# Kernel tuning notes

Measured on AMD Instinct MI355X. Metric: run time of the kernel, lower is better.

Reference implementation:

```python
import jax, jax.numpy as jnp
from jax import lax
import numpy as np

N_LAYERS = 2
HIDDEN = 1024
N_STOCKS = 1024
LB, UB = 0.0, 0.2
REBAL_ITERS = 32  # fixed upper bound; loop converges in 1-2 iters in practice


def setup_inputs() -> dict:
    key = jax.random.key(0)
    ks = jax.random.split(key, 20)
    B, T = 512, 128
    inp = {"x": jax.random.normal(ks[0], (B, T, N_STOCKS), dtype=jnp.float32)}
    k = 1
    for l in range(N_LAYERS):
        in_dim = N_STOCKS if l == 0 else HIDDEN
        s = 1.0 / np.sqrt(HIDDEN)
        inp[f"w_ih_{l}"] = jax.random.uniform(ks[k], (3 * HIDDEN, in_dim), minval=-s, maxval=s); k += 1
        inp[f"w_hh_{l}"] = jax.random.uniform(ks[k], (3 * HIDDEN, HIDDEN), minval=-s, maxval=s); k += 1
        inp[f"b_ih_{l}"] = jax.random.uniform(ks[k], (3 * HIDDEN,), minval=-s, maxval=s); k += 1
        inp[f"b_hh_{l}"] = jax.random.uniform(ks[k], (3 * HIDDEN,), minval=-s, maxval=s); k += 1
    s = 1.0 / np.sqrt(HIDDEN)
    inp["fc_w"] = jax.random.uniform(ks[k], (N_STOCKS, HIDDEN), minval=-s, maxval=s); k += 1
    inp["fc_b"] = jax.random.uniform(ks[k], (N_STOCKS,), minval=-s, maxval=s)
    return inp


def _gru_layer(x, w_ih, w_hh, b_ih, b_hh):
    # x: [B,T,D] -> hidden sequence [B,T,H]; PyTorch GRU cell math
    B, T, _ = x.shape
    H = w_hh.shape[1]
    x_proj = jnp.einsum('btd,gd->btg', x, w_ih) + b_ih  # [B,T,3H]

    def step(h, xp):
        hp = h @ w_hh.T + b_hh
        xr, xz, xn = jnp.split(xp, 3, axis=-1)
        hr, hz, hn = jnp.split(hp, 3, axis=-1)
        r = jax.nn.sigmoid(xr + hr)
        z = jax.nn.sigmoid(xz + hz)
        n = jnp.tanh(xn + r * hn)
        h_new = (1.0 - z) * n + z * h
        return h_new, h_new

    h0 = jnp.zeros((B, H), x.dtype)
    _, hs = lax.scan(step, h0, jnp.swapaxes(x_proj, 0, 1))  # [T,B,H]
    return jnp.swapaxes(hs, 0, 1)


def _rebalance(w, lb, ub, n_iters=REBAL_ITERS):
    # Batched version of the iterative capped-simplex redistribution loop.
    old = w
    wc = jnp.clip(w, lb, ub)
    done = jnp.zeros((w.shape[0],), dtype=bool)

    def body(state, _):
        old, wc, done = state
        leftover = jnp.sum(old - wc, axis=-1, keepdims=True)            # [B,1]
        mask = wc != ub                                                  # nominees
        num = jnp.sum(mask, axis=-1)                                     # [B]
        nom_sum = jnp.sum(jnp.where(mask, wc, 0.0), axis=-1, keepdims=True)
        gift = leftover * wc / jnp.where(nom_sum == 0.0, 1.0, nom_sum)
        wc_new = jnp.where(mask, wc + gift, wc)
        no_nom = num == 0
        over = jnp.any(wc_new > ub, axis=-1)
        new_done = done | no_nom | (~over)
        wc_next = jnp.where(no_nom[:, None], wc,
                            jnp.where(over[:, None], jnp.clip(wc_new, lb, ub), wc_new))
        old_next = jnp.where(no_nom[:, None], old, wc_new)
        wc_out = jnp.where(done[:, None], wc, wc_next)
        old_out = jnp.where(done[:, None], old, old_next)
        return (old_out, wc_out, new_done), None

    (_, wc, _), _ = lax.scan(body, (old, wc, done), None, length=n_iters)
    return wc


def reference(x, w_ih_0, w_hh_0, b_ih_0, b_hh_0, w_ih_1, w_hh_1, b_ih_1, b_hh_1, fc_w, fc_b):
    h = _gru_layer(x, w_ih_0, w_hh_0, b_ih_0, b_hh_0)
    h = _gru_layer(h, w_ih_1, w_hh_1, b_ih_1, b_hh_1)
    h_t = h[:, -1, :]                                   # last time step [B,H]
    logit = h_t @ fc_w.T + fc_b                         # dropout is identity in eval
    logit = jax.nn.silu(logit)
    probs = jax.nn.softmax(logit, axis=-1)
    return _rebalance(probs, LB, UB)
```

## Files before the change

### kernel.cpp

```cpp
#include <hip/hip_runtime.h>
#include <hip/hip_bf16.h>
#include <stdint.h>

#define BB 512
#define TT 128
#define DD 1024
#define HH 1024
#define G3 3072
#define TC 32
#define NCH (TT/TC)
#define NRING 33

typedef __bf16 bft;
typedef __bf16 bf16x8 __attribute__((ext_vector_type(8)));
typedef float f32x4 __attribute__((ext_vector_type(4)));

__device__ __forceinline__ void gl_lds16(const bft* g, void* lds_base_uniform) {
  __builtin_amdgcn_global_load_lds(
      (const __attribute__((address_space(1))) void*)g,
      (__attribute__((address_space(3))) void*)lds_base_uniform,
      16, 0, 0);
}

__device__ __forceinline__ void st_wt_bf16(bft* p, float v) {
  bft h = (bft)v;
  union { bft h; unsigned short u; } cv; cv.h = h;
  unsigned int uv = cv.u;
  asm volatile("global_store_short %0, %1, off sc0 sc1" :: "v"(p), "v"(uv) : "memory");
}
__device__ __forceinline__ void st_wt_f32(float* p, float v) {
  asm volatile("global_store_dword %0, %1, off sc0 sc1" :: "v"(p), "v"(v) : "memory");
}
__device__ __forceinline__ void st_wt_u32(int* p, int v) {
  asm volatile("global_store_dword %0, %1, off sc0 sc1" :: "v"(p), "v"(v) : "memory");
}
__device__ __forceinline__ int ld_co_u32(const int* p) {
  int v;
  asm volatile("global_load_dword %0, %1, off sc0 sc1\n\ts_waitcnt vmcnt(0)"
               : "=v"(v) : "v"(p) : "memory");
  return v;
}

__global__ void k_cvt(const float* __restrict__ in, bft* __restrict__ out, long n) {
  long i = ((long)blockIdx.x * blockDim.x + threadIdx.x) * 8;
  long stride = (long)gridDim.x * blockDim.x * 8;
  for (; i < n; i += stride) {
    float4 a = *(const float4*)(in + i);
    float4 b = *(const float4*)(in + i + 4);
    bf16x8 r;
    r[0] = (bft)a.x; r[1] = (bft)a.y; r[2] = (bft)a.z; r[3] = (bft)a.w;
    r[4] = (bft)b.x; r[5] = (bft)b.y; r[6] = (bft)b.z; r[7] = (bft)b.w;
    *(bf16x8*)(out + i) = r;
  }
}

template<int AMODE, int EPI>
__launch_bounds__(256)
__global__ void k_gemm(const void* __restrict__ Ap, long lda,
                       const bft* __restrict__ W, long ldw,
                       const float* __restrict__ bias,
                       void* __restrict__ Cout, long ldc,
                       int t0, int K) {
  __shared__ unsigned char sm[32768];
  const int tid  = threadIdx.x;
  const int lane = tid & 63;
  const int wid  = tid >> 6;
  const int m0 = blockIdx.y * 128;
  const int n0 = blockIdx.x * 128;
  const int wm = wid >> 1, wn = wid & 1;

  f32x4 acc[4][4] = {};

  for (int k0 = 0; k0 < K; k0 += 64) {
    if (AMODE == 1) {
      const float* Af = (const float*)Ap;
#pragma unroll
      for (int s = 0; s < 4; ++s) {
        int seg = wid * 4 + s;
        int row = seg * 8 + (lane >> 3);
        int mr = m0 + row;
        long grow = (long)(mr >> 5) * TT + t0 + (mr & 31);
        const float* src = Af + grow * lda + k0 + (lane & 7) * 8;
        float4 a  = *(const float4*)src;
        float4 b2 = *(const float4*)(src + 4);
        bf16x8 r;
        r[0] = (bft)a.x;  r[1] = (bft)a.y;  r[2] = (bft)a.z;  r[3] = (bft)a.w;
        r[4] = (bft)b2.x; r[5] = (bft)b2.y; r[6] = (bft)b2.z; r[7] = (bft)b2.w;
        *(bf16x8*)(sm + seg * 1024 + (lane >> 3) * 128 +
                   (((lane & 7) * 16) ^ ((row & 7) << 4))) = r;
      }
    } else {
      const bft* Ab = (const bft*)Ap;
#pragma unroll
      for (int s = 0; s < 4; ++s) {
        int seg = wid * 4 + s;
        int row = seg * 8 + (lane >> 3);
        int cbs = ((lane & 7) * 16) ^ ((row & 7) << 4);
        int mr = m0 + row;
        long grow;
        if (AMODE == 0) grow = mr;
        else { int sl = t0 + (mr & 31); if (sl >= NRING) sl -= NRING;
               grow = (long)sl * BB + (mr >> 5); }
        gl_lds16(Ab + grow * lda + k0 + (cbs >> 1), sm + seg * 1024);
      }
    }
#pragma unroll
    for (int s = 0; s < 4; ++s) {
      int seg = wid * 4 + s;
      int row = seg * 8 + (lane >> 3);
      int cbs = ((lane & 7) * 16) ^ ((row & 7) << 4);
      gl_lds16(W + (long)(n0 + row) * ldw + k0 + (cbs >> 1), sm + 16384 + seg * 1024);
    }
    __syncthreads();
#pragma unroll
    for (int ks = 0; ks < 2; ++ks) {
      int kb = ks * 64 + (lane >> 4) * 16;
      bf16x8 aF[4], bF[4];
#pragma unroll
      for (int mi = 0; mi < 4; ++mi) {
        int row = wm * 64 + mi * 16 + (lane & 15);
        aF[mi] = *(const bf16x8*)(sm + row * 128 + (kb ^ ((row & 7) << 4)));
      }
#pragma unroll
      for (int ni = 0; ni < 4; ++ni) {
        int row = wn * 64 + ni * 16 + (lane & 15);
        bF[ni] = *(const bf16x8*)(sm + 16384 + row * 128 + (kb ^ ((row & 7) << 4)));
      }
#pragma unroll
      for (int mi = 0; mi < 4; ++mi)
#pragma unroll
        for (int ni = 0; ni < 4; ++ni)
          acc[mi][ni] = __builtin_amdgcn_mfma_f32_16x16x32_bf16(aF[mi], bF[ni], acc[mi][ni], 0, 0, 0);
    }
    __syncthreads();
  }

#pragma unroll
  for (int mi = 0; mi < 4; ++mi)
#pragma unroll
    for (int ni = 0; ni < 4; ++ni) {
      int col = n0 + wn * 64 + ni * 16 + (lane & 15);
      float bv = bias[col];
#pragma unroll
      for (int r = 0; r < 4; ++r) {
        long row = m0 + wm * 64 + mi * 16 + (lane >> 4) * 4 + r;
        float v = acc[mi][ni][r] + bv;
        if (EPI == 0) {
          ((bft*)Cout)[row * ldc + col] = (bft)v;
        } else {
          ((float*)Cout)[row * ldc + col] = v / (1.f + expf(-v));
        }
      }
    }
}

__launch_bounds__(256, 1)
__global__ void k_persist(const bft* __restrict__ whh, const float* __restrict__ bhh,
                          const bft* __restrict__ xp,
                          bft* __restrict__ ring,
                          float* __restrict__ hfc, int* __restrict__ flags,
                          int t0s, int first, int pbase) {
  __shared__ unsigned char sm[163840];
  unsigned char* smW = sm;
  unsigned char* smA = sm + 98304;

  const int tid  = threadIdx.x;
  const int lane = tid & 63;
  const int wid  = tid >> 6;
  const int bid  = blockIdx.x;
  const int xcd = bid & 7, loc = bid >> 3;
  const int mt = xcd >> 1;
  const int nt = (xcd & 1) * 32 + loc;
  const int j0 = nt * 16;
  const int m0 = mt * 128;
  const int j  = j0 + (lane & 15);
  int* gflags = flags + mt * 64;

#pragma unroll
  for (int s8 = 0; s8 < 24; ++s8) {
    int s = wid * 24 + s8;
    int row = s >> 1;
    int half = s & 1;
    int hb = half * 1024 + lane * 16;
    int sb = hb ^ ((row & 7) << 4);
    long grow = (long)(row >> 4) * 1024 + j0 + (row & 15);
    gl_lds16(whh + grow * 1024 + (sb >> 1), smW + s * 1024);
  }
  asm volatile("s_waitcnt vmcnt(0)" ::: "memory");
  __builtin_amdgcn_s_barrier();

  const float br = bhh[j], bz = bhh[1024 + j], bn = bhh[2048 + j];

  auto stageA = [&](const bft* base, int k0, int bufsel) {
    unsigned char* dst = smA + bufsel * 16384;
#pragma unroll
    for (int si = 0; si < 4; ++si) {
      int seg = wid * 4 + si;
      int row = seg * 8 + (lane >> 3);
      int cb = ((lane & 7) * 16) ^ ((row & 7) << 4);
      gl_lds16(base + (long)(m0 + row) * DD + k0 + (cb >> 1), dst + seg * 1024);
    }
  };

  float xg[3][2][4];
  float hp[2][4];

  auto prefXG = [&](int s) {
#pragma unroll
    for (int mi = 0; mi < 2; ++mi)
#pragma unroll
      for (int r = 0; r < 4; ++r) {
        long b = m0 + wid * 32 + mi * 16 + (lane >> 4) * 4 + r;
        long xrow = (b * TC + s) * (long)G3 + j;
        xg[0][mi][r] = (float)xp[xrow];
        xg[1][mi][r] = (float)xp[xrow + 1024];
        xg[2][mi][r] = (float)xp[xrow + 2048];
      }
  };

  prefXG(0);
  if (first) {
#pragma unroll
    for (int mi = 0; mi < 2; ++mi)
#pragma unroll
      for (int r = 0; r < 4; ++r) hp[mi][r] = 0.f;
  } else {
#pragma unroll
    for (int mi = 0; mi < 2; ++mi)
#pragma unroll
      for (int r = 0; r < 4; ++r) {
        long b = m0 + wid * 32 + mi * 16 + (lane >> 4) * 4 + r;
        hp[mi][r] = hfc[b * HH + j];
      }
  }
  __builtin_amdgcn_sched_barrier(0);

  for (int s = 0; s < TC; ++s) {
    if (s) {
      int target = pbase + s;
      if (tid < 64) {
        const int* fp = gflags + tid;
        while (ld_co_u32(fp) < target) __builtin_amdgcn_s_sleep(2);
      }
      __syncthreads();
    }

    int sl = t0s + s; if (sl >= NRING) sl -= NRING;
    int psl = sl ? sl - 1 : NRING - 1;

    f32x4 acc[3][2] = {};
    if (!(first && s == 0)) {
      const bft* Ab = ring + (long)psl * (BB * (long)DD);
      stageA(Ab, 0, 0);
      stageA(Ab, 64, 1);
      stageA(Ab, 128, 2);
#pragma unroll
      for (int k = 0; k < 16; ++k) {
        __builtin_amdgcn_s_barrier();
        if (k < 13) stageA(Ab, (k + 3) * 64, (k + 3) & 3);
        if (k < 13)       asm volatile("s_waitcnt vmcnt(12)" ::: "memory");
        else if (k == 13) asm volatile("s_waitcnt vmcnt(8)" ::: "memory");
        else if (k == 14) asm volatile("s_waitcnt vmcnt(4)" ::: "memory");
        else              asm volatile("s_waitcnt vmcnt(0)" ::: "memory");
        __builtin_amdgcn_s_barrier();
        __builtin_amdgcn_sched_barrier(0);
        const unsigned char* Abuf = smA + (k & 3) * 16384;
#pragma unroll
        for (int ks = 0; ks < 2; ++ks) {
          int kb = ks * 64 + (lane >> 4) * 16;
          bf16x8 aF[2], bF[3];
#pragma unroll
          for (int mi = 0; mi < 2; ++mi) {
            int row = wid * 32 + mi * 16 + (lane & 15);
            aF[mi] = *(const bf16x8*)(Abuf + row * 128 + (kb ^ ((row & 7) << 4)));
          }
#pragma unroll
          for (int g = 0; g < 3; ++g) {
            int wrow = g * 16 + (lane & 15);
            bF[g] = *(const bf16x8*)(smW + wrow * 2048 + ((k * 128 + kb) ^ ((wrow & 7) << 4)));
          }
#pragma unroll
          for (int g = 0; g < 3; ++g)
#pragma unroll
            for (int mi = 0; mi < 2; ++mi)
              acc[g][mi] = __builtin_amdgcn_mfma_f32_16x16x32_bf16(aF[mi], bF[g], acc[g][mi], 0, 0, 0);
        }
      }
    }

    bft* outp = ring + (long)sl * (BB * (long)DD);
#pragma unroll
    for (int mi = 0; mi < 2; ++mi)
#pragma unroll
      for (int r = 0; r < 4; ++r) {
        long b = m0 + wid * 32 + mi * 16 + (lane >> 4) * 4 + r;
        float hr = acc[0][mi][r] + br;
        float hz = acc[1][mi][r] + bz;
        float hn = acc[2][mi][r] + bn;
        float rg = 1.f / (1.f + expf(-(xg[0][mi][r] + hr)));
        float zg = 1.f / (1.f + expf(-(xg[1][mi][r] + hz)));
        float ng = tanhf(xg[2][mi][r] + rg * hn);
        float hv = (1.f - zg) * ng + zg * hp[mi][r];
        hp[mi][r] = hv;
        st_wt_bf16(outp + b * DD + j, hv);
        if (s == TC - 1) st_wt_f32(hfc + b * HH + j, hv);
      }

    __syncthreads();
    if (s < TC - 1) {
      if (tid == 0) st_wt_u32(gflags + nt, pbase + s + 1);
      prefXG(s + 1);
      __builtin_amdgcn_sched_barrier(0);
    }
  }
}

__device__ __forceinline__ float blk_sum(float v, float* red, int tid) {
#pragma unroll
  for (int o = 32; o; o >>= 1) v += __shfl_xor(v, o);
  if ((tid & 63) == 0) red[tid >> 6] = v;
  __syncthreads();
  v = red[0] + red[1] + red[2] + red[3];
  __syncthreads();
  return v;
}
__device__ __forceinline__ float blk_max(float v, float* red, int tid) {
#pragma unroll
  for (int o = 32; o; o >>= 1) v = fmaxf(v, __shfl_xor(v, o));
  if ((tid & 63) == 0) red[tid >> 6] = v;
  __syncthreads();
  v = fmaxf(fmaxf(red[0], red[1]), fmaxf(red[2], red[3]));
  __syncthreads();
  return v;
}

__launch_bounds__(256)
__global__ void k_smrebal(const float* __restrict__ logits, float* __restrict__ out) {
  __shared__ float red[4];
  const int tid = threadIdx.x;
  const long row = blockIdx.x;
  const float ub = 0.2f, lb = 0.0f;
  float4 lv = *(const float4*)(logits + row * 1024 + tid * 4);

  float m = fmaxf(fmaxf(lv.x, lv.y), fmaxf(lv.z, lv.w));
  m = blk_max(m, red, tid);
  float e[4] = {expf(lv.x - m), expf(lv.y - m), expf(lv.z - m), expf(lv.w - m)};
  float S = blk_sum(e[0] + e[1] + e[2] + e[3], red, tid);

  float old_[4], wc[4];
#pragma unroll
  for (int k = 0; k < 4; ++k) {
    float p = e[k] / S;
    old_[k] = p;
    wc[k] = fminf(fmaxf(p, lb), ub);
  }
  bool done = false;
  for (int it = 0; it < 32 && !done; ++it) {
    float d3 = 0.f, cnt = 0.f, nsum = 0.f;
#pragma unroll
    for (int k = 0; k < 4; ++k) {
      d3 += old_[k] - wc[k];
      bool mk = (wc[k] != ub);
      cnt += mk ? 1.f : 0.f;
      nsum += mk ? wc[k] : 0.f;
    }
    float leftover = blk_sum(d3, red, tid);
    float num = blk_sum(cnt, red, tid);
    float nom_sum = blk_sum(nsum, red, tid);
    float denom = (nom_sum == 0.f) ? 1.f : nom_sum;
    float wcn[4], mx = -1e30f;
#pragma unroll
    for (int k = 0; k < 4; ++k) {
      bool mk = (wc[k] != ub);
      wcn[k] = mk ? wc[k] + leftover * wc[k] / denom : wc[k];
      mx = fmaxf(mx, wcn[k]);
    }
    float gmx = blk_max(mx, red, tid);
    bool no_nom = (num == 0.f);
    bool over = (gmx > ub);
#pragma unroll
    for (int k = 0; k < 4; ++k) {
      float nxt = no_nom ? wc[k] : (over ? fminf(fmaxf(wcn[k], lb), ub) : wcn[k]);
      float oldn = no_nom ? old_[k] : wcn[k];
      wc[k] = nxt;
      old_[k] = oldn;
    }
    done = no_nom || !over;
  }
#pragma unroll
  for (int k = 0; k < 4; ++k) out[row * 1024 + tid * 4 + k] = wc[k];
}

extern "C" void kernel_launch(void* const* d_in, const int* in_sizes, int n_in,
                              void* d_out, int out_size, void* d_ws, size_t ws_size,
                              hipStream_t stream) {
  const float* x      = (const float*)d_in[0];
  const float* wih[2] = {(const float*)d_in[1], (const float*)d_in[5]};
  const float* whh[2] = {(const float*)d_in[2], (const float*)d_in[6]};
  const float* bih[2] = {(const float*)d_in[3], (const float*)d_in[7]};
  const float* bhh[2] = {(const float*)d_in[4], (const float*)d_in[8]};
  const float* fcw    = (const float*)d_in[9];
  const float* fcb    = (const float*)d_in[10];
  float* outp = (float*)d_out;

  unsigned char* ws = (unsigned char*)d_ws;
  size_t off = 0;
  auto alloc = [&](size_t bytes) -> void* {
    void* p = ws + off;
    off += (bytes + 255) & ~(size_t)255;
    return p;
  };
  bft* wihb0   = (bft*)alloc((size_t)G3 * DD * 2);
  bft* whhb0   = (bft*)alloc((size_t)G3 * HH * 2);
  bft* wihb1   = (bft*)alloc((size_t)G3 * HH * 2);
  bft* whhb1   = (bft*)alloc((size_t)G3 * HH * 2);
  bft* fcwb    = (bft*)alloc((size_t)1024 * 1024 * 2);
  bft* xp      = (bft*)alloc((size_t)BB * TC * G3 * 2);
  bft* ring0   = (bft*)alloc((size_t)NRING * BB * DD * 2);
  bft* ring1   = (bft*)alloc((size_t)NRING * BB * DD * 2);
  float* hfc0  = (float*)alloc((size_t)BB * HH * 4);
  float* hfc1  = (float*)alloc((size_t)BB * HH * 4);
  int* flags   = (int*)alloc(1024);
  float* logits= (float*)alloc((size_t)BB * 1024 * 4);
  if (off > ws_size) return;

  hipMemsetAsync(flags, 0, 1024, stream);

  k_cvt<<<dim3(1536), dim3(256), 0, stream>>>(wih[0], wihb0, (long)G3 * DD);
  k_cvt<<<dim3(1536), dim3(256), 0, stream>>>(whh[0], whhb0, (long)G3 * HH);
  k_cvt<<<dim3(1536), dim3(256), 0, stream>>>(wih[1], wihb1, (long)G3 * HH);
  k_cvt<<<dim3(1536), dim3(256), 0, stream>>>(whh[1], whhb1, (long)G3 * HH);
  k_cvt<<<dim3(512),  dim3(256), 0, stream>>>(fcw, fcwb, (long)1024 * 1024);

  for (int c = 0; c < NCH; ++c) {
    int t0 = c * TC;
    int t0s = t0 % NRING;
    int first = (c == 0) ? 1 : 0;
    k_gemm<1, 0><<<dim3(G3 / 128, (BB * TC) / 128), 256, 0, stream>>>(
        x, DD, wihb0, DD, bih[0], xp, G3, t0, DD);
    k_persist<<<dim3(256), dim3(256), 0, stream>>>(
        whhb0, bhh[0], xp, ring0, hfc0, flags, t0s, first, (2 * c) * TC);
    k_gemm<2, 0><<<dim3(G3 / 128, (BB * TC) / 128), 256, 0, stream>>>(
        ring0, DD, wihb1, DD, bih[1], xp, G3, t0s, DD);
    k_persist<<<dim3(256), dim3(256), 0, stream>>>(
        whhb1, bhh[1], xp, ring1, hfc1, flags, t0s, first, (2 * c + 1) * TC);
  }
  const bft* hfin = ring1 + (size_t)((TT - 1) % NRING) * BB * DD;
  k_gemm<0, 1><<<dim3(1024 / 128, BB / 128), 256, 0, stream>>>(
      hfin, DD, fcwb, HH, fcb, logits, 1024, 0, HH);
  k_smrebal<<<dim3(BB), 256, 0, stream>>>(logits, outp);
}
```

Baseline: 3.081 ms.

## Hold r/z recurrent weights in registers and use fast exp/rcp gate math

The persistent GRU kernel now keeps the r and z gate slices of W_hh in VGPRs per lane (64 bf16x8 vectors) and stages only the n-gate slice in LDS. This cuts LDS from 160KB to 96KB and removes two of three LDS B-fragment reads per MFMA step. The gate nonlinearities also switch from expf/tanhf to raw v_exp_f32/v_rcp_f32, which is cheaper but less accurate. The large register footprint (256 VGPRs for weights) risks spilling or tighter register pressure.

```diff
diff --git a/kernel.cpp b/kernel.cpp
--- a/kernel.cpp
+++ b/kernel.cpp
@@ -40,6 +40,14 @@
                : "=v"(v) : "v"(p) : "memory");
   return v;
 }
+
+__device__ __forceinline__ float fexp2(float x) {
+  float r; asm("v_exp_f32 %0, %1" : "=v"(r) : "v"(x)); return r;
+}
+__device__ __forceinline__ float frcp(float x) {
+  float r; asm("v_rcp_f32 %0, %1" : "=v"(r) : "v"(x)); return r;
+}
+#define LOG2E 1.44269504f
 
 __global__ void k_cvt(const float* __restrict__ in, bft* __restrict__ out, long n) {
   long i = ((long)blockIdx.x * blockDim.x + threadIdx.x) * 8;
@@ -160,9 +168,9 @@
                           bft* __restrict__ ring,
                           float* __restrict__ hfc, int* __restrict__ flags,
                           int t0s, int first, int pbase) {
-  __shared__ unsigned char sm[163840];
+  __shared__ unsigned char sm[98304];
   unsigned char* smW = sm;
-  unsigned char* smA = sm + 98304;
+  unsigned char* smA = sm + 32768;
 
   const int tid  = threadIdx.x;
   const int lane = tid & 63;
@@ -177,14 +185,25 @@
   int* gflags = flags + mt * 64;
 
 #pragma unroll
-  for (int s8 = 0; s8 < 24; ++s8) {
-    int s = wid * 24 + s8;
+  for (int s8 = 0; s8 < 8; ++s8) {
+    int s = wid * 8 + s8;
     int row = s >> 1;
     int half = s & 1;
     int hb = half * 1024 + lane * 16;
     int sb = hb ^ ((row & 7) << 4);
-    long grow = (long)(row >> 4) * 1024 + j0 + (row & 15);
+    long grow = (long)(2 * 1024 + j0 + row);
     gl_lds16(whh + grow * 1024 + (sb >> 1), smW + s * 1024);
+  }
+
+  bf16x8 wrz[2][16][2];
+#pragma unroll
+  for (int g = 0; g < 2; ++g) {
+    const bft* wbase = whh + (((long)g * 1024 + j) << 10) + ((lane >> 4) * 8);
+#pragma unroll
+    for (int k = 0; k < 16; ++k)
+#pragma unroll
+      for (int ks = 0; ks < 2; ++ks)
+        wrz[g][k][ks] = *(const bf16x8*)(wbase + k * 64 + ks * 32);
   }
   asm volatile("s_waitcnt vmcnt(0)" ::: "memory");
   __builtin_amdgcn_s_barrier();
@@ -268,22 +287,21 @@
 #pragma unroll
         for (int ks = 0; ks < 2; ++ks) {
           int kb = ks * 64 + (lane >> 4) * 16;
-          bf16x8 aF[2], bF[3];
+          bf16x8 aF[2];
 #pragma unroll
           for (int mi = 0; mi < 2; ++mi) {
             int row = wid * 32 + mi * 16 + (lane & 15);
             aF[mi] = *(const bf16x8*)(Abuf + row * 128 + (kb ^ ((row & 7) << 4)));
           }
-#pragma unroll
-          for (int g = 0; g < 3; ++g) {
-            int wrow = g * 16 + (lane & 15);
-            bF[g] = *(const bf16x8*)(smW + wrow * 2048 + ((k * 128 + kb) ^ ((wrow & 7) << 4)));
+          int wrow = lane & 15;
+          bf16x8 bFn = *(const bf16x8*)(smW + wrow * 2048 +
+                                        ((k * 128 + kb) ^ ((wrow & 7) << 4)));
+#pragma unroll
+          for (int mi = 0; mi < 2; ++mi) {
+            acc[0][mi] = __builtin_amdgcn_mfma_f32_16x16x32_bf16(aF[mi], wrz[0][k][ks], acc[0][mi], 0, 0, 0);
+            acc[1][mi] = __builtin_amdgcn_mfma_f32_16x16x32_bf16(aF[mi], wrz[1][k][ks], acc[1][mi], 0, 0, 0);
+            acc[2][mi] = __builtin_amdgcn_mfma_f32_16x16x32_bf16(aF[mi], bFn,           acc[2][mi], 0, 0, 0);
           }
-#pragma unroll
-          for (int g = 0; g < 3; ++g)
-#pragma unroll
-            for (int mi = 0; mi < 2; ++mi)
-              acc[g][mi] = __builtin_amdgcn_mfma_f32_16x16x32_bf16(aF[mi], bF[g], acc[g][mi], 0, 0, 0);
         }
       }
     }
@@ -297,9 +315,10 @@
         float hr = acc[0][mi][r] + br;
         float hz = acc[1][mi][r] + bz;
         float hn = acc[2][mi][r] + bn;
-        float rg = 1.f / (1.f + expf(-(xg[0][mi][r] + hr)));
-        float zg = 1.f / (1.f + expf(-(xg[1][mi][r] + hz)));
-        float ng = tanhf(xg[2][mi][r] + rg * hn);
+        float rg = frcp(1.f + fexp2(-LOG2E * (xg[0][mi][r] + hr)));
+        float zg = frcp(1.f + fexp2(-LOG2E * (xg[1][mi][r] + hz)));
+        float e2 = fexp2(2.f * LOG2E * (xg[2][mi][r] + rg * hn));
+        float ng = 1.f - 2.f * frcp(e2 + 1.f);
         float hv = (1.f - zg) * ng + zg * hp[mi][r];
         hp[mi][r] = hv;
         st_wt_bf16(outp + b * DD + j, hv);
```

After: 4.235 ms. +37.5%, slower.
